# Optimization experiments

Measured on AMD Instinct MI355X. Metric: run time of the kernel, lower is better.

## Reference

```python
import jax, jax.numpy as jnp
import numpy as np

NQ = 8
DIM = 2 ** NQ  # 256 amplitudes
HALF_PI = float(np.pi / 2)

CNOT_M = jnp.array([[1, 0, 0, 0], [0, 1, 0, 0], [0, 0, 0, 1], [0, 0, 1, 0]], dtype=jnp.complex64)
SWAP_M = jnp.array([[1, 0, 0, 0], [0, 0, 1, 0], [0, 1, 0, 0], [0, 0, 0, 1]], dtype=jnp.complex64)

# PauliZ sign vectors per wire; wire 0 is the most-significant bit (PennyLane convention)
_bits = (np.arange(DIM)[None, :] >> (NQ - 1 - np.arange(NQ))[:, None]) & 1
ZSIGNS = jnp.asarray(1.0 - 2.0 * _bits, dtype=jnp.float32)  # [NQ, DIM]


def _rx(t):
    c = jnp.cos(0.5 * t).astype(jnp.complex64)
    s = (-1j * jnp.sin(0.5 * t)).astype(jnp.complex64)
    return jnp.stack([jnp.stack([c, s]), jnp.stack([s, c])])


def _ry(t):
    c = jnp.cos(0.5 * t).astype(jnp.complex64)
    s = jnp.sin(0.5 * t).astype(jnp.complex64)
    return jnp.stack([jnp.stack([c, -s]), jnp.stack([s, c])])


def _rz(t):
    e0 = jnp.exp(-0.5j * t).astype(jnp.complex64)
    e1 = jnp.exp(0.5j * t).astype(jnp.complex64)
    z = jnp.zeros((), jnp.complex64)
    return jnp.stack([jnp.stack([e0, z]), jnp.stack([z, e1])])


def _ixx(t):
    c = jnp.cos(0.5 * t).astype(jnp.complex64)
    s = (-1j * jnp.sin(0.5 * t)).astype(jnp.complex64)
    z = jnp.zeros((), jnp.complex64)
    return jnp.stack([jnp.stack([c, z, z, s]), jnp.stack([z, c, s, z]),
                      jnp.stack([z, s, c, z]), jnp.stack([s, z, z, c])])


def _apply_1q(psi, U, w):
    # psi: [B] + [2]*NQ ; apply 2x2 U on wire w
    psi = jnp.moveaxis(psi, 1 + w, -1)
    psi = psi @ U.T
    return jnp.moveaxis(psi, -1, 1 + w)


def _apply_2q(psi, U, w1, w2):
    # apply 4x4 U on wires (w1, w2); w1 is the more-significant wire of U
    psi = jnp.moveaxis(psi, (1 + w1, 1 + w2), (-2, -1))
    shp = psi.shape
    psi = (psi.reshape(shp[:-2] + (4,)) @ U.T).reshape(shp)
    return jnp.moveaxis(psi, (-2, -1), (1 + w1, 1 + w2))


def _edges_from_coupling(coupling):
    # Mirrors the torch code: threshold min-max normalized coupling at 0.5.
    # This is a non-differentiable, data-dependent circuit-structure decision,
    # so it is resolved on concrete values (as the Python ifs do in torch).
    c = np.asarray(jax.device_get(coupling), dtype=np.float64)
    cn = (c - c.min()) / (c.max() - c.min())
    adj = cn > 0.5
    return [(i, j) for i in range(NQ) for j in range(i + 1, NQ) if adj[i, j]]


def _conv(psi, i, j, p):
    psi = _apply_1q(psi, _rz(jnp.float32(-HALF_PI)), j)
    psi = _apply_2q(psi, CNOT_M, j, i)  # CNOT control=j target=i
    psi = _apply_1q(psi, _rz(p[0]), i)
    psi = _apply_1q(psi, _ry(p[1]), j)
    psi = _apply_2q(psi, CNOT_M, i, j)
    psi = _apply_1q(psi, _ry(p[2]), j)
    psi = _apply_2q(psi, CNOT_M, j, i)
    psi = _apply_1q(psi, _rz(jnp.float32(HALF_PI)), i)
    return psi


def _pool(psi, i, j, p):
    psi = _apply_1q(psi, _rz(jnp.float32(-HALF_PI)), j)
    psi = _apply_2q(psi, CNOT_M, j, i)
    psi = _apply_1q(psi, _rz(p[0]), i)
    psi = _apply_1q(psi, _ry(p[1]), j)
    psi = _apply_2q(psi, CNOT_M, i, j)
    psi = _apply_1q(psi, _ry(p[2]), j)
    return psi


def _circuit(x, weights, coupling, edges):
    B = x.shape[0]
    # AmplitudeEmbedding(normalize=True)
    psi = (x / jnp.linalg.norm(x, axis=1, keepdims=True)).astype(jnp.complex64)
    psi = psi.reshape((B,) + (2,) * NQ)
    for i in range(NQ):
        psi = _apply_1q(psi, _rx(weights[i]), i)
        psi = _apply_1q(psi, _ry(weights[i + NQ]), i)
        psi = _apply_1q(psi, _rz(weights[i + 2 * NQ]), i)
    for i in range(NQ):
        for j in range(i + 1, NQ):
            psi = _apply_2q(psi, _ixx(coupling[i, j]), i, j)
    widx = 3 * NQ
    for (i, j) in edges:
        nonadjacent = abs(i - j) != 1
        if nonadjacent:
            psi = _apply_2q(psi, SWAP_M, i, j)
        psi = _conv(psi, i, j, weights[widx:widx + 3])
        psi = _pool(psi, i, j, weights[widx + 3:widx + 6])
        widx += 6
        if nonadjacent:
            psi = _apply_2q(psi, SWAP_M, i, j)
    psi_f = psi.reshape(B, DIM)
    probs = psi_f.real ** 2 + psi_f.imag ** 2  # [B, DIM]
    return probs @ ZSIGNS.T  # [B, NQ] expval(PauliZ(i))


def setup_inputs() -> dict:
    B = 65536
    key = jax.random.key(0)
    k1, k2, k3 = jax.random.split(key, 3)
    x = jax.random.normal(k1, (B, DIM), dtype=jnp.float32)
    weights = jax.random.normal(k2, (3 * NQ + 6 * 28,), dtype=jnp.float32)  # 192: max edges = C(8,2)=28
    coupling = jax.random.normal(k3, (NQ, NQ), dtype=jnp.float32)
    return {"x": x, "weights": weights, "coupling": coupling}


def reference(x, weights, coupling):
    edges = _edges_from_coupling(coupling)
    return _circuit(x, weights, coupling, edges)
```

## Files before the change

### kernel.cpp

```cpp
#include <hip/hip_runtime.h>

#define HP 1.57079632679489662f

typedef float f32x4 __attribute__((ext_vector_type(4)));
typedef short sh4 __attribute__((ext_vector_type(4)));
typedef __bf16 bf16x8 __attribute__((ext_vector_type(8)));

__device__ __forceinline__ unsigned short f2bf(float f) {
  unsigned int u = __builtin_bit_cast(unsigned int, f);
  u += 0x7fffu + ((u >> 16) & 1u);
  return (unsigned short)(u >> 16);
}

__device__ __forceinline__ void rowswap4(float (&mr)[4][4], float (&mi)[4][4], int a, int b) {
#pragma unroll
  for (int c = 0; c < 4; c++) {
    float tr = mr[a][c]; mr[a][c] = mr[b][c]; mr[b][c] = tr;
    float ti = mi[a][c]; mi[a][c] = mi[b][c]; mi[b][c] = ti;
  }
}

__device__ __forceinline__ void absorb_rz(float (&mr)[4][4], float (&mi)[4][4], float t, int bitpos) {
  float ch = cosf(0.5f * t), sh = sinf(0.5f * t);
#pragma unroll
  for (int r = 0; r < 4; r++) {
    float ph = ((r >> bitpos) & 1) ? sh : -sh;
#pragma unroll
    for (int c = 0; c < 4; c++) {
      float ar = mr[r][c], ai = mi[r][c];
      mr[r][c] = ch * ar - ph * ai;
      mi[r][c] = ch * ai + ph * ar;
    }
  }
}

__device__ __forceinline__ void absorb_ry(float (&mr)[4][4], float (&mi)[4][4], float t, int bitpos) {
  float ch = cosf(0.5f * t), sh = sinf(0.5f * t);
#pragma unroll
  for (int r = 0; r < 4; r++) {
    if ((r >> bitpos) & 1) continue;
    int rb = r | (1 << bitpos);
#pragma unroll
    for (int c = 0; c < 4; c++) {
      float ar = mr[r][c], ai = mi[r][c];
      float br = mr[rb][c], bi = mi[rb][c];
      mr[r][c]  = ch * ar - sh * br;  mi[r][c]  = ch * ai - sh * bi;
      mr[rb][c] = sh * ar + ch * br;  mi[rb][c] = sh * ai + ch * bi;
    }
  }
}


__global__ __launch_bounds__(256) void build_u_kernel(const float* __restrict__ wt,
                                                      const float* __restrict__ coup,
                                                      void* __restrict__ wsv) {
  unsigned char* Ub = (unsigned char*)wsv + 4096;
  const int c = blockIdx.x;
  const int tid = threadIdx.x;

  __shared__ float2 s[256];
  __shared__ float Q1s[64];
  __shared__ float E4s[28 * 32];
  __shared__ int metas[57];

  {
    double mn = 1e300, mx = -1e300;
    for (int k = 0; k < 64; k++) {
      double v = (double)coup[k];
      mn = v < mn ? v : mn;
      mx = v > mx ? v : mx;
    }
    int cnt = 0, myi = -1, myj = -1;
    for (int i = 0; i < 8; i++)
      for (int j = i + 1; j < 8; j++) {
        double cn = ((double)coup[i * 8 + j] - mn) / (mx - mn);
        if (cn > 0.5) {
          if (cnt == tid) { myi = i; myj = j; }
          cnt++;
        }
      }
    if (tid == 0) metas[0] = cnt;

    if (tid < 8) {
      float tx = wt[tid], ty = wt[8 + tid], tz = wt[16 + tid];
      float cx = cosf(0.5f * tx), sx = sinf(0.5f * tx);
      float cy = cosf(0.5f * ty), sy = sinf(0.5f * ty);
      float cz = cosf(0.5f * tz), sz = sinf(0.5f * tz);
      float m00r = cy * cx,  m00i = sy * sx;
      float m01r = -sy * cx, m01i = -cy * sx;
      float m10r = sy * cx,  m10i = -cy * sx;
      float m11r = cy * cx,  m11i = -sy * sx;
      float* q = Q1s + tid * 8;
      q[0] = cz * m00r + sz * m00i; q[1] = cz * m00i - sz * m00r;
      q[2] = cz * m01r + sz * m01i; q[3] = cz * m01i - sz * m01r;
      q[4] = cz * m10r - sz * m10i; q[5] = cz * m10i + sz * m10r;
      q[6] = cz * m11r - sz * m11i; q[7] = cz * m11i + sz * m11r;
    }

    if (tid < cnt && tid < 28) {
      float mr[4][4], mi[4][4];
#pragma unroll
      for (int r = 0; r < 4; r++)
#pragma unroll
        for (int cc = 0; cc < 4; cc++) { mr[r][cc] = (r == cc) ? 1.f : 0.f; mi[r][cc] = 0.f; }

      bool nonadj = (myj - myi) != 1;
      int wb = 24 + 6 * tid;

      if (nonadj) rowswap4(mr, mi, 1, 2);
      absorb_rz(mr, mi, -HP, 0);
      rowswap4(mr, mi, 1, 3);
      absorb_rz(mr, mi, wt[wb + 0], 1);
      absorb_ry(mr, mi, wt[wb + 1], 0);
      rowswap4(mr, mi, 2, 3);
      absorb_ry(mr, mi, wt[wb + 2], 0);
      rowswap4(mr, mi, 1, 3);
      absorb_rz(mr, mi, HP, 1);
      absorb_rz(mr, mi, -HP, 0);
      rowswap4(mr, mi, 1, 3);
      absorb_rz(mr, mi, wt[wb + 3], 1);
      absorb_ry(mr, mi, wt[wb + 4], 0);
      rowswap4(mr, mi, 2, 3);
      absorb_ry(mr, mi, wt[wb + 5], 0);
      if (nonadj) rowswap4(mr, mi, 1, 2);

      float* e = E4s + tid * 32;
#pragma unroll
      for (int r = 0; r < 4; r++)
#pragma unroll
        for (int cc = 0; cc < 4; cc++) {
          e[(r * 4 + cc) * 2]     = mr[r][cc];
          e[(r * 4 + cc) * 2 + 1] = mi[r][cc];
        }
      metas[1 + 2 * tid] = myi;
      metas[2 + 2 * tid] = myj;
    }
  }

  s[tid] = make_float2(tid == c ? 1.f : 0.f, 0.f);
  __syncthreads();

  for (int wi = 0; wi < 8; wi++) {
    const float* M = Q1s + wi * 8;
    int p = 7 - wi;
    float2 a0 = s[tid & ~(1 << p)];
    float2 a1 = s[tid | (1 << p)];
    int b = (tid >> p) & 1;
    float m0r = M[(b * 2 + 0) * 2], m0i = M[(b * 2 + 0) * 2 + 1];
    float m1r = M[(b * 2 + 1) * 2], m1i = M[(b * 2 + 1) * 2 + 1];
    float nr = m0r * a0.x - m0i * a0.y + m1r * a1.x - m1i * a1.y;
    float ni = m0r * a0.y + m0i * a0.x + m1r * a1.y + m1i * a1.x;
    __syncthreads();
    s[tid] = make_float2(nr, ni);
    __syncthreads();
  }

  for (int i = 0; i < 8; i++)
    for (int j = i + 1; j < 8; j++) {
      float t = coup[i * 8 + j];
      float ch = cosf(0.5f * t), sn = sinf(0.5f * t);
      int mask = (1 << (7 - i)) | (1 << (7 - j));
      float2 a = s[tid];
      float2 b = s[tid ^ mask];
      __syncthreads();
      s[tid] = make_float2(ch * a.x + sn * b.y, ch * a.y - sn * b.x);
      __syncthreads();
    }

  int ne = metas[0];
  for (int e = 0; e < ne; e++) {
    int i = metas[1 + 2 * e], j = metas[2 + 2 * e];
    int p1 = 7 - i, p2 = 7 - j;
    int m1 = 1 << p1, m2 = 1 << p2;
    int b = ((tid >> p1) & 1) * 2 + ((tid >> p2) & 1);
    int base = tid & ~(m1 | m2);
    float2 a0 = s[base];
    float2 a1 = s[base | m2];
    float2 a2 = s[base | m1];
    float2 a3 = s[base | m1 | m2];
    const float* M = E4s + e * 32 + b * 8;
    float nr = M[0] * a0.x - M[1] * a0.y + M[2] * a1.x - M[3] * a1.y
             + M[4] * a2.x - M[5] * a2.y + M[6] * a3.x - M[7] * a3.y;
    float ni = M[0] * a0.y + M[1] * a0.x + M[2] * a1.y + M[3] * a1.x
             + M[4] * a2.y + M[5] * a2.x + M[6] * a3.y + M[7] * a3.x;
    __syncthreads();
    s[tid] = make_float2(nr, ni);
    __syncthreads();
  }

  {
    int ks = c >> 5, kc = c & 31;
    int sb = (kc >> 4) & 1, lg2 = (kc >> 2) & 3, ii = kc & 3;
    int p = (lg2 + tid) & 3;
    unsigned char* base = Ub + (size_t)ks * 32768 + (size_t)(2 * tid) * 64 + p * 16 + sb * 8 + ii * 2;
    *(unsigned short*)(base)      = f2bf(s[tid].x);
    *(unsigned short*)(base + 64) = f2bf(s[tid].y);
  }
}

#define MFMA_STEP(KS, AREG)                                                              \
  {                                                                                      \
    uint4 bq[4];                                                                         \
    _Pragma("unroll")                                                                    \
    for (int nf = 0; nf < 4; nf++) {                                                     \
      const int n = nf * 16 + lm;                                                        \
      int byte = (n * 512 + (KS) * 64 + lg * 16) ^ ((n & 7) << 4);                       \
      bq[nf] = *reinterpret_cast<const uint4*>(&smem[byte]);                             \
    }                                                                                    \
    __builtin_amdgcn_s_setprio(1);                                                       \
    _Pragma("unroll")                                                                    \
    for (int mf = 0; mf < 4; mf++) {                                                     \
      const sh4 alo = __builtin_bit_cast(sh4, make_uint2(AREG[mf].x, AREG[mf].y));       \
      const sh4 ahi = __builtin_bit_cast(sh4, make_uint2(AREG[mf].z, AREG[mf].w));       \
      _Pragma("unroll")                                                                  \
      for (int nf = 0; nf < 4; nf++) {                                                   \
        const sh4 blo = __builtin_bit_cast(sh4, make_uint2(bq[nf].x, bq[nf].y));         \
        const sh4 bhi = __builtin_bit_cast(sh4, make_uint2(bq[nf].z, bq[nf].w));         \
        acc[mf][nf] = __builtin_amdgcn_mfma_f32_16x16x16bf16_1k(alo, blo, acc[mf][nf], 0, 0, 0); \
        acc[mf][nf] = __builtin_amdgcn_mfma_f32_16x16x16bf16_1k(ahi, bhi, acc[mf][nf], 0, 0, 0); \
      }                                                                                  \
    }                                                                                    \
    __builtin_amdgcn_s_setprio(0);                                                       \
  }

__global__ __launch_bounds__(512, 4) void gemm_l2(const float* __restrict__ x,
                                                  const void* __restrict__ wsv,
                                                  float* __restrict__ out) {
  const unsigned char* Ub = (const unsigned char*)wsv + 4096;
  __shared__ __align__(16) unsigned char smem[32768];

  const int tid = threadIdx.x;
  const int tile = blockIdx.x;
  const int wv = tid >> 6;
  const int lane = tid & 63;
  const int lm = lane & 15;
  const int lg = lane >> 4;

  const unsigned char* abase[4];
#pragma unroll
  for (int mf = 0; mf < 4; mf++) {
    const int m = wv * 64 + mf * 16 + lm;
    const int p = (lg + (m >> 1)) & 3;
    abase[mf] = Ub + (size_t)m * 64 + p * 16;
  }
  uint4 aP[4], aQ[4];
#pragma unroll
  for (int mf = 0; mf < 4; mf++) aP[mf] = *reinterpret_cast<const uint4*>(abase[mf]);

  {
    const int rl = tid >> 3;
    const int seg = tid & 7;
    const float4* xs = (const float4*)(x + (size_t)(tile * 64 + rl) * 256 + seg * 32);
    float4 v[8];
    float ss = 0.f;
#pragma unroll
    for (int i = 0; i < 8; i++) {
      v[i] = xs[i];
      ss += v[i].x * v[i].x + v[i].y * v[i].y + v[i].z * v[i].z + v[i].w * v[i].w;
    }
    ss += __shfl_xor(ss, 1);
    ss += __shfl_xor(ss, 2);
    ss += __shfl_xor(ss, 4);
    float inv = 1.0f / sqrtf(ss);
    const float* vf = (const float*)v;
#pragma unroll
    for (int u = 0; u < 4; u++) {
      bf16x8 w;
#pragma unroll
      for (int j = 0; j < 8; j++)
        w[j] = (__bf16)(vf[16 * (j >> 2) + 4 * u + (j & 3)] * inv);
      uint4 pack = __builtin_bit_cast(uint4, w);
      int byte = (rl * 512 + seg * 64 + u * 16) ^ ((rl & 7) << 4);
      *reinterpret_cast<uint4*>(&smem[byte]) = pack;
    }
  }

  f32x4 acc[4][4] = {};
  __syncthreads();

#pragma unroll
  for (int kk = 0; kk < 4; kk++) {
#pragma unroll
    for (int mf = 0; mf < 4; mf++)
      aQ[mf] = *reinterpret_cast<const uint4*>(abase[mf] + (size_t)(2 * kk + 1) * 32768);
    MFMA_STEP(2 * kk, aP);
    if (kk < 3) {
#pragma unroll
      for (int mf = 0; mf < 4; mf++)
        aP[mf] = *reinterpret_cast<const uint4*>(abase[mf] + (size_t)(2 * kk + 2) * 32768);
    }
    MFMA_STEP(2 * kk + 1, aQ);
  }
  __syncthreads();

  float pq[4][8];
#pragma unroll
  for (int nf = 0; nf < 4; nf++) {
    float T = 0.f, S7 = 0.f, S4 = 0.f, S3 = 0.f;
#pragma unroll
    for (int mf = 0; mf < 4; mf++) {
      f32x4 a = acc[mf][nf];
      float p0 = a[0] * a[0] + a[1] * a[1];
      float p1 = a[2] * a[2] + a[3] * a[3];
      float sp = p0 + p1, d = p0 - p1;
      T += sp;
      S7 += d;
      S4 += (mf & 1) ? -sp : sp;
      S3 += (mf & 2) ? -sp : sp;
    }
    pq[nf][7] = S7;
    pq[nf][6] = (lg & 1) ? -T : T;
    pq[nf][5] = (lg & 2) ? -T : T;
    pq[nf][4] = S4;
    pq[nf][3] = S3;
    pq[nf][2] = (wv & 1) ? -T : T;
    pq[nf][1] = (wv & 2) ? -T : T;
    pq[nf][0] = (wv & 4) ? -T : T;
  }
#pragma unroll
  for (int nf = 0; nf < 4; nf++)
#pragma unroll
    for (int k = 0; k < 8; k++) {
      pq[nf][k] += __shfl_xor(pq[nf][k], 16);
      pq[nf][k] += __shfl_xor(pq[nf][k], 32);
    }

  float* part = (float*)smem;
  if (lg == 0) {
#pragma unroll
    for (int nf = 0; nf < 4; nf++) {
      float* dst = part + (wv * 64 + nf * 16 + lm) * 8;
#pragma unroll
      for (int k = 0; k < 8; k++) dst[k] = pq[nf][k];
    }
  }
  __syncthreads();
  {
    int b = tid >> 3, q = tid & 7;
    float v2 = 0.f;
#pragma unroll
    for (int w2 = 0; w2 < 8; w2++) v2 += part[(w2 * 64 + b) * 8 + q];
    out[(size_t)(tile * 64 + b) * 8 + q] = v2;
  }
}

extern "C" void kernel_launch(void* const* d_in, const int* in_sizes, int n_in,
                              void* d_out, int out_size, void* d_ws, size_t ws_size,
                              hipStream_t stream) {
  const float* x    = (const float*)d_in[0];
  const float* wt   = (const float*)d_in[1];
  const float* coup = (const float*)d_in[2];
  float* out = (float*)d_out;

  build_u_kernel<<<256, 256, 0, stream>>>(wt, coup, d_ws);
  gemm_l2<<<1024, 512, 0, stream>>>(x, d_ws, out);
}
```

Baseline: 58.57 us.

## Run unitary build in one wave with shuffles; rotate K-chunk order in GEMM

New measurement: 70.69 us. +20.7%, slower.

```diff
diff --git a/kernel.cpp b/kernel.cpp
--- a/kernel.cpp
+++ b/kernel.cpp
@@ -51,14 +51,13 @@
 }
 
 
-__global__ __launch_bounds__(256) void build_u_kernel(const float* __restrict__ wt,
-                                                      const float* __restrict__ coup,
-                                                      void* __restrict__ wsv) {
+__global__ __launch_bounds__(64) void build_u_wave(const float* __restrict__ wt,
+                                                   const float* __restrict__ coup,
+                                                   void* __restrict__ wsv) {
   unsigned char* Ub = (unsigned char*)wsv + 4096;
   const int c = blockIdx.x;
-  const int tid = threadIdx.x;
-
-  __shared__ float2 s[256];
+  const int lane = threadIdx.x;
+
   __shared__ float Q1s[64];
   __shared__ float E4s[28 * 32];
   __shared__ int metas[57];
@@ -75,14 +74,14 @@
       for (int j = i + 1; j < 8; j++) {
         double cn = ((double)coup[i * 8 + j] - mn) / (mx - mn);
         if (cn > 0.5) {
-          if (cnt == tid) { myi = i; myj = j; }
+          if (cnt == lane) { myi = i; myj = j; }
           cnt++;
         }
       }
-    if (tid == 0) metas[0] = cnt;
-
-    if (tid < 8) {
-      float tx = wt[tid], ty = wt[8 + tid], tz = wt[16 + tid];
+    if (lane == 0) metas[0] = cnt;
+
+    if (lane < 8) {
+      float tx = wt[lane], ty = wt[8 + lane], tz = wt[16 + lane];
       float cx = cosf(0.5f * tx), sx = sinf(0.5f * tx);
       float cy = cosf(0.5f * ty), sy = sinf(0.5f * ty);
       float cz = cosf(0.5f * tz), sz = sinf(0.5f * tz);
@@ -90,14 +89,14 @@
       float m01r = -sy * cx, m01i = -cy * sx;
       float m10r = sy * cx,  m10i = -cy * sx;
       float m11r = cy * cx,  m11i = -sy * sx;
-      float* q = Q1s + tid * 8;
+      float* q = Q1s + lane * 8;
       q[0] = cz * m00r + sz * m00i; q[1] = cz * m00i - sz * m00r;
       q[2] = cz * m01r + sz * m01i; q[3] = cz * m01i - sz * m01r;
       q[4] = cz * m10r - sz * m10i; q[5] = cz * m10i + sz * m10r;
       q[6] = cz * m11r - sz * m11i; q[7] = cz * m11i + sz * m11r;
     }
 
-    if (tid < cnt && tid < 28) {
+    if (lane < cnt && lane < 28) {
       float mr[4][4], mi[4][4];
 #pragma unroll
       for (int r = 0; r < 4; r++)
@@ -105,7 +104,7 @@
         for (int cc = 0; cc < 4; cc++) { mr[r][cc] = (r == cc) ? 1.f : 0.f; mi[r][cc] = 0.f; }
 
       bool nonadj = (myj - myi) != 1;
-      int wb = 24 + 6 * tid;
+      int wb = 24 + 6 * lane;
 
       if (nonadj) rowswap4(mr, mi, 1, 2);
       absorb_rz(mr, mi, -HP, 0);
@@ -124,7 +123,7 @@
       absorb_ry(mr, mi, wt[wb + 5], 0);
       if (nonadj) rowswap4(mr, mi, 1, 2);
 
-      float* e = E4s + tid * 32;
+      float* e = E4s + lane * 32;
 #pragma unroll
       for (int r = 0; r < 4; r++)
 #pragma unroll
@@ -132,27 +131,51 @@
           e[(r * 4 + cc) * 2]     = mr[r][cc];
           e[(r * 4 + cc) * 2 + 1] = mi[r][cc];
         }
-      metas[1 + 2 * tid] = myi;
-      metas[2 + 2 * tid] = myj;
-    }
-  }
-
-  s[tid] = make_float2(tid == c ? 1.f : 0.f, 0.f);
+      metas[1 + 2 * lane] = myi;
+      metas[2 + 2 * lane] = myj;
+    }
+  }
   __syncthreads();
+
+  float2 st[4];
+#pragma unroll
+  for (int q = 0; q < 4; q++)
+    st[q] = make_float2((q * 64 + lane) == c ? 1.f : 0.f, 0.f);
+
+  auto partner = [&](int M, float2 (&par)[4]) {
+    const int qm = M >> 6, lm = M & 63;
+    float2 t0, t1, t2, t3;
+    if (qm == 0)      { t0 = st[0]; t1 = st[1]; t2 = st[2]; t3 = st[3]; }
+    else if (qm == 1) { t0 = st[1]; t1 = st[0]; t2 = st[3]; t3 = st[2]; }
+    else if (qm == 2) { t0 = st[2]; t1 = st[3]; t2 = st[0]; t3 = st[1]; }
+    else              { t0 = st[3]; t1 = st[2]; t2 = st[1]; t3 = st[0]; }
+    if (lm) {
+      t0.x = __shfl_xor(t0.x, lm); t0.y = __shfl_xor(t0.y, lm);
+      t1.x = __shfl_xor(t1.x, lm); t1.y = __shfl_xor(t1.y, lm);
+      t2.x = __shfl_xor(t2.x, lm); t2.y = __shfl_xor(t2.y, lm);
+      t3.x = __shfl_xor(t3.x, lm); t3.y = __shfl_xor(t3.y, lm);
+    }
+    par[0] = t0; par[1] = t1; par[2] = t2; par[3] = t3;
+  };
 
   for (int wi = 0; wi < 8; wi++) {
     const float* M = Q1s + wi * 8;
-    int p = 7 - wi;
-    float2 a0 = s[tid & ~(1 << p)];
-    float2 a1 = s[tid | (1 << p)];
-    int b = (tid >> p) & 1;
-    float m0r = M[(b * 2 + 0) * 2], m0i = M[(b * 2 + 0) * 2 + 1];
-    float m1r = M[(b * 2 + 1) * 2], m1i = M[(b * 2 + 1) * 2 + 1];
-    float nr = m0r * a0.x - m0i * a0.y + m1r * a1.x - m1i * a1.y;
-    float ni = m0r * a0.y + m0i * a0.x + m1r * a1.y + m1i * a1.x;
-    __syncthreads();
-    s[tid] = make_float2(nr, ni);
-    __syncthreads();
+    const int p = 7 - wi;
+    float2 par[4];
+    partner(1 << p, par);
+    float m00r = M[0], m00i = M[1], m01r = M[2], m01i = M[3];
+    float m10r = M[4], m10i = M[5], m11r = M[6], m11i = M[7];
+#pragma unroll
+    for (int q = 0; q < 4; q++) {
+      int b = ((q * 64 + lane) >> p) & 1;
+      float2 own = st[q], pr = par[q];
+      float2 x0 = b ? pr : own;
+      float2 x1 = b ? own : pr;
+      float c0r = b ? m10r : m00r, c0i = b ? m10i : m00i;
+      float c1r = b ? m11r : m01r, c1i = b ? m11i : m01i;
+      st[q].x = c0r * x0.x - c0i * x0.y + c1r * x1.x - c1i * x1.y;
+      st[q].y = c0r * x0.y + c0i * x0.x + c1r * x1.y + c1i * x1.x;
+    }
   }
 
   for (int i = 0; i < 8; i++)
@@ -160,11 +183,13 @@
       float t = coup[i * 8 + j];
       float ch = cosf(0.5f * t), sn = sinf(0.5f * t);
       int mask = (1 << (7 - i)) | (1 << (7 - j));
-      float2 a = s[tid];
-      float2 b = s[tid ^ mask];
-      __syncthreads();
-      s[tid] = make_float2(ch * a.x + sn * b.y, ch * a.y - sn * b.x);
-      __syncthreads();
+      float2 par[4];
+      partner(mask, par);
+#pragma unroll
+      for (int q = 0; q < 4; q++) {
+        float2 own = st[q], pr = par[q];
+        st[q] = make_float2(ch * own.x + sn * pr.y, ch * own.y - sn * pr.x);
+      }
     }
 
   int ne = metas[0];
@@ -172,29 +197,39 @@
     int i = metas[1 + 2 * e], j = metas[2 + 2 * e];
     int p1 = 7 - i, p2 = 7 - j;
     int m1 = 1 << p1, m2 = 1 << p2;
-    int b = ((tid >> p1) & 1) * 2 + ((tid >> p2) & 1);
-    int base = tid & ~(m1 | m2);
-    float2 a0 = s[base];
-    float2 a1 = s[base | m2];
-    float2 a2 = s[base | m1];
-    float2 a3 = s[base | m1 | m2];
-    const float* M = E4s + e * 32 + b * 8;
-    float nr = M[0] * a0.x - M[1] * a0.y + M[2] * a1.x - M[3] * a1.y
-             + M[4] * a2.x - M[5] * a2.y + M[6] * a3.x - M[7] * a3.y;
-    float ni = M[0] * a0.y + M[1] * a0.x + M[2] * a1.y + M[3] * a1.x
-             + M[4] * a2.y + M[5] * a2.x + M[6] * a3.y + M[7] * a3.x;
-    __syncthreads();
-    s[tid] = make_float2(nr, ni);
-    __syncthreads();
+    float2 pa2[4], pa1[4], pa12[4];
+    partner(m2, pa2);
+    partner(m1, pa1);
+    partner(m1 | m2, pa12);
+    const float* E = E4s + e * 32;
+#pragma unroll
+    for (int q = 0; q < 4; q++) {
+      int r = q * 64 + lane;
+      int b = ((r >> p1) & 1) * 2 + ((r >> p2) & 1);
+      float nr = 0.f, ni = 0.f;
+      { float Mr = E[(b * 4 + b) * 2], Mi = E[(b * 4 + b) * 2 + 1];
+        nr += Mr * st[q].x - Mi * st[q].y; ni += Mr * st[q].y + Mi * st[q].x; }
+      { int t2 = b ^ 1; float Mr = E[(b * 4 + t2) * 2], Mi = E[(b * 4 + t2) * 2 + 1];
+        nr += Mr * pa2[q].x - Mi * pa2[q].y; ni += Mr * pa2[q].y + Mi * pa2[q].x; }
+      { int t2 = b ^ 2; float Mr = E[(b * 4 + t2) * 2], Mi = E[(b * 4 + t2) * 2 + 1];
+        nr += Mr * pa1[q].x - Mi * pa1[q].y; ni += Mr * pa1[q].y + Mi * pa1[q].x; }
+      { int t2 = b ^ 3; float Mr = E[(b * 4 + t2) * 2], Mi = E[(b * 4 + t2) * 2 + 1];
+        nr += Mr * pa12[q].x - Mi * pa12[q].y; ni += Mr * pa12[q].y + Mi * pa12[q].x; }
+      st[q] = make_float2(nr, ni);
+    }
   }
 
   {
     int ks = c >> 5, kc = c & 31;
     int sb = (kc >> 4) & 1, lg2 = (kc >> 2) & 3, ii = kc & 3;
-    int p = (lg2 + tid) & 3;
-    unsigned char* base = Ub + (size_t)ks * 32768 + (size_t)(2 * tid) * 64 + p * 16 + sb * 8 + ii * 2;
-    *(unsigned short*)(base)      = f2bf(s[tid].x);
-    *(unsigned short*)(base + 64) = f2bf(s[tid].y);
+#pragma unroll
+    for (int q = 0; q < 4; q++) {
+      int r = q * 64 + lane;
+      int p = (lg2 + r) & 3;
+      unsigned char* base = Ub + (size_t)ks * 32768 + (size_t)(2 * r) * 64 + p * 16 + sb * 8 + ii * 2;
+      *(unsigned short*)(base)      = f2bf(st[q].x);
+      *(unsigned short*)(base + 64) = f2bf(st[q].y);
+    }
   }
 }
 
@@ -235,6 +270,7 @@
   const int lane = tid & 63;
   const int lm = lane & 15;
   const int lg = lane >> 4;
+  const int rot = (blockIdx.x >> 3) & 7;
 
   const unsigned char* abase[4];
 #pragma unroll
@@ -245,7 +281,8 @@
   }
   uint4 aP[4], aQ[4];
 #pragma unroll
-  for (int mf = 0; mf < 4; mf++) aP[mf] = *reinterpret_cast<const uint4*>(abase[mf]);
+  for (int mf = 0; mf < 4; mf++)
+    aP[mf] = *reinterpret_cast<const uint4*>(abase[mf] + (size_t)rot * 32768);
 
   {
     const int rl = tid >> 3;
@@ -280,16 +317,19 @@
 
 #pragma unroll
   for (int kk = 0; kk < 4; kk++) {
+    const int c0 = (2 * kk + rot) & 7;
+    const int c1 = (2 * kk + 1 + rot) & 7;
 #pragma unroll
     for (int mf = 0; mf < 4; mf++)
-      aQ[mf] = *reinterpret_cast<const uint4*>(abase[mf] + (size_t)(2 * kk + 1) * 32768);
-    MFMA_STEP(2 * kk, aP);
+      aQ[mf] = *reinterpret_cast<const uint4*>(abase[mf] + (size_t)c1 * 32768);
+    MFMA_STEP(c0, aP);
     if (kk < 3) {
+      const int c2 = (2 * kk + 2 + rot) & 7;
 #pragma unroll
       for (int mf = 0; mf < 4; mf++)
-        aP[mf] = *reinterpret_cast<const uint4*>(abase[mf] + (size_t)(2 * kk + 2) * 32768);
-    }
-    MFMA_STEP(2 * kk + 1, aQ);
+        aP[mf] = *reinterpret_cast<const uint4*>(abase[mf] + (size_t)c2 * 32768);
+    }
+    MFMA_STEP(c1, aQ);
   }
   __syncthreads();
 
@@ -352,6 +392,6 @@
   const float* coup = (const float*)d_in[2];
   float* out = (float*)d_out;
 
-  build_u_kernel<<<256, 256, 0, stream>>>(wt, coup, d_ws);
+  build_u_wave<<<256, 64, 0, stream>>>(wt, coup, d_ws);
   gemm_l2<<<1024, 512, 0, stream>>>(x, d_ws, out);
 }
```

## Process two batch tiles per GEMM block and build unitary with single-wave blocks

Applied to the files above, without the earlier changes.

Result: slower. 74.33 us (+26.9%).

```diff
diff --git a/kernel.cpp b/kernel.cpp
--- a/kernel.cpp
+++ b/kernel.cpp
@@ -51,12 +51,12 @@
 }
 
 
-__global__ __launch_bounds__(256) void build_u_kernel(const float* __restrict__ wt,
-                                                      const float* __restrict__ coup,
-                                                      void* __restrict__ wsv) {
+__global__ __launch_bounds__(64) void build_u_wave(const float* __restrict__ wt,
+                                                   const float* __restrict__ coup,
+                                                   void* __restrict__ wsv) {
   unsigned char* Ub = (unsigned char*)wsv + 4096;
   const int c = blockIdx.x;
-  const int tid = threadIdx.x;
+  const int lane = threadIdx.x;
 
   __shared__ float2 s[256];
   __shared__ float Q1s[64];
@@ -75,14 +75,14 @@
       for (int j = i + 1; j < 8; j++) {
         double cn = ((double)coup[i * 8 + j] - mn) / (mx - mn);
         if (cn > 0.5) {
-          if (cnt == tid) { myi = i; myj = j; }
+          if (cnt == lane) { myi = i; myj = j; }
           cnt++;
         }
       }
-    if (tid == 0) metas[0] = cnt;
-
-    if (tid < 8) {
-      float tx = wt[tid], ty = wt[8 + tid], tz = wt[16 + tid];
+    if (lane == 0) metas[0] = cnt;
+
+    if (lane < 8) {
+      float tx = wt[lane], ty = wt[8 + lane], tz = wt[16 + lane];
       float cx = cosf(0.5f * tx), sx = sinf(0.5f * tx);
       float cy = cosf(0.5f * ty), sy = sinf(0.5f * ty);
       float cz = cosf(0.5f * tz), sz = sinf(0.5f * tz);
@@ -90,14 +90,14 @@
       float m01r = -sy * cx, m01i = -cy * sx;
       float m10r = sy * cx,  m10i = -cy * sx;
       float m11r = cy * cx,  m11i = -sy * sx;
-      float* q = Q1s + tid * 8;
+      float* q = Q1s + lane * 8;
       q[0] = cz * m00r + sz * m00i; q[1] = cz * m00i - sz * m00r;
       q[2] = cz * m01r + sz * m01i; q[3] = cz * m01i - sz * m01r;
       q[4] = cz * m10r - sz * m10i; q[5] = cz * m10i + sz * m10r;
       q[6] = cz * m11r - sz * m11i; q[7] = cz * m11i + sz * m11r;
     }
 
-    if (tid < cnt && tid < 28) {
+    if (lane < cnt && lane < 28) {
       float mr[4][4], mi[4][4];
 #pragma unroll
       for (int r = 0; r < 4; r++)
@@ -105,7 +105,7 @@
         for (int cc = 0; cc < 4; cc++) { mr[r][cc] = (r == cc) ? 1.f : 0.f; mi[r][cc] = 0.f; }
 
       bool nonadj = (myj - myi) != 1;
-      int wb = 24 + 6 * tid;
+      int wb = 24 + 6 * lane;
 
       if (nonadj) rowswap4(mr, mi, 1, 2);
       absorb_rz(mr, mi, -HP, 0);
@@ -124,7 +124,7 @@
       absorb_ry(mr, mi, wt[wb + 5], 0);
       if (nonadj) rowswap4(mr, mi, 1, 2);
 
-      float* e = E4s + tid * 32;
+      float* e = E4s + lane * 32;
 #pragma unroll
       for (int r = 0; r < 4; r++)
 #pragma unroll
@@ -132,27 +132,31 @@
           e[(r * 4 + cc) * 2]     = mr[r][cc];
           e[(r * 4 + cc) * 2 + 1] = mi[r][cc];
         }
-      metas[1 + 2 * tid] = myi;
-      metas[2 + 2 * tid] = myj;
-    }
-  }
-
-  s[tid] = make_float2(tid == c ? 1.f : 0.f, 0.f);
-  __syncthreads();
+      metas[1 + 2 * lane] = myi;
+      metas[2 + 2 * lane] = myj;
+    }
+  }
+
+#pragma unroll
+  for (int q = 0; q < 4; q++)
+    s[q * 64 + lane] = make_float2((q * 64 + lane) == c ? 1.f : 0.f, 0.f);
 
   for (int wi = 0; wi < 8; wi++) {
-    const float* M = Q1s + wi * 8;
-    int p = 7 - wi;
-    float2 a0 = s[tid & ~(1 << p)];
-    float2 a1 = s[tid | (1 << p)];
-    int b = (tid >> p) & 1;
-    float m0r = M[(b * 2 + 0) * 2], m0i = M[(b * 2 + 0) * 2 + 1];
-    float m1r = M[(b * 2 + 1) * 2], m1i = M[(b * 2 + 1) * 2 + 1];
-    float nr = m0r * a0.x - m0i * a0.y + m1r * a1.x - m1i * a1.y;
-    float ni = m0r * a0.y + m0i * a0.x + m1r * a1.y + m1i * a1.x;
-    __syncthreads();
-    s[tid] = make_float2(nr, ni);
-    __syncthreads();
+    const int p = 7 - wi;
+    const int m = 1 << p;
+    float2 nw[4];
+#pragma unroll
+    for (int q = 0; q < 4; q++) {
+      int r = q * 64 + lane;
+      int b = (r >> p) & 1;
+      float2 a0 = s[r & ~m];
+      float2 a1 = s[r | m];
+      float4 Mv = *reinterpret_cast<const float4*>(&Q1s[wi * 8 + b * 4]);
+      nw[q].x = Mv.x * a0.x - Mv.y * a0.y + Mv.z * a1.x - Mv.w * a1.y;
+      nw[q].y = Mv.x * a0.y + Mv.y * a0.x + Mv.z * a1.y + Mv.w * a1.x;
+    }
+#pragma unroll
+    for (int q = 0; q < 4; q++) s[q * 64 + lane] = nw[q];
   }
 
   for (int i = 0; i < 8; i++)
@@ -160,11 +164,16 @@
       float t = coup[i * 8 + j];
       float ch = cosf(0.5f * t), sn = sinf(0.5f * t);
       int mask = (1 << (7 - i)) | (1 << (7 - j));
-      float2 a = s[tid];
-      float2 b = s[tid ^ mask];
-      __syncthreads();
-      s[tid] = make_float2(ch * a.x + sn * b.y, ch * a.y - sn * b.x);
-      __syncthreads();
+      float2 nw[4];
+#pragma unroll
+      for (int q = 0; q < 4; q++) {
+        int r = q * 64 + lane;
+        float2 own = s[r];
+        float2 pr = s[r ^ mask];
+        nw[q] = make_float2(ch * own.x + sn * pr.y, ch * own.y - sn * pr.x);
+      }
+#pragma unroll
+      for (int q = 0; q < 4; q++) s[q * 64 + lane] = nw[q];
     }
 
   int ne = metas[0];
@@ -172,39 +181,49 @@
     int i = metas[1 + 2 * e], j = metas[2 + 2 * e];
     int p1 = 7 - i, p2 = 7 - j;
     int m1 = 1 << p1, m2 = 1 << p2;
-    int b = ((tid >> p1) & 1) * 2 + ((tid >> p2) & 1);
-    int base = tid & ~(m1 | m2);
-    float2 a0 = s[base];
-    float2 a1 = s[base | m2];
-    float2 a2 = s[base | m1];
-    float2 a3 = s[base | m1 | m2];
-    const float* M = E4s + e * 32 + b * 8;
-    float nr = M[0] * a0.x - M[1] * a0.y + M[2] * a1.x - M[3] * a1.y
-             + M[4] * a2.x - M[5] * a2.y + M[6] * a3.x - M[7] * a3.y;
-    float ni = M[0] * a0.y + M[1] * a0.x + M[2] * a1.y + M[3] * a1.x
-             + M[4] * a2.y + M[5] * a2.x + M[6] * a3.y + M[7] * a3.x;
-    __syncthreads();
-    s[tid] = make_float2(nr, ni);
-    __syncthreads();
+    float2 nw[4];
+#pragma unroll
+    for (int q = 0; q < 4; q++) {
+      int r = q * 64 + lane;
+      int b = ((r >> p1) & 1) * 2 + ((r >> p2) & 1);
+      int base = r & ~(m1 | m2);
+      float2 a0 = s[base];
+      float2 a1 = s[base | m2];
+      float2 a2 = s[base | m1];
+      float2 a3 = s[base | m1 | m2];
+      float4 M01 = *reinterpret_cast<const float4*>(&E4s[e * 32 + b * 8]);
+      float4 M23 = *reinterpret_cast<const float4*>(&E4s[e * 32 + b * 8 + 4]);
+      nw[q].x = M01.x * a0.x - M01.y * a0.y + M01.z * a1.x - M01.w * a1.y
+              + M23.x * a2.x - M23.y * a2.y + M23.z * a3.x - M23.w * a3.y;
+      nw[q].y = M01.x * a0.y + M01.y * a0.x + M01.z * a1.y + M01.w * a1.x
+              + M23.x * a2.y + M23.y * a2.x + M23.z * a3.y + M23.w * a3.x;
+    }
+#pragma unroll
+    for (int q = 0; q < 4; q++) s[q * 64 + lane] = nw[q];
   }
 
   {
     int ks = c >> 5, kc = c & 31;
     int sb = (kc >> 4) & 1, lg2 = (kc >> 2) & 3, ii = kc & 3;
-    int p = (lg2 + tid) & 3;
-    unsigned char* base = Ub + (size_t)ks * 32768 + (size_t)(2 * tid) * 64 + p * 16 + sb * 8 + ii * 2;
-    *(unsigned short*)(base)      = f2bf(s[tid].x);
-    *(unsigned short*)(base + 64) = f2bf(s[tid].y);
-  }
-}
-
-#define MFMA_STEP(KS, AREG)                                                              \
+#pragma unroll
+    for (int q = 0; q < 4; q++) {
+      int r = q * 64 + lane;
+      int p = (lg2 + r) & 3;
+      unsigned char* base = Ub + (size_t)ks * 32768 + (size_t)(2 * r) * 64 + p * 16 + sb * 8 + ii * 2;
+      float2 a = s[r];
+      *(unsigned short*)(base)      = f2bf(a.x);
+      *(unsigned short*)(base + 64) = f2bf(a.y);
+    }
+  }
+}
+
+#define MFMA_STEP(PSIOFF, KS, AREG)                                                      \
   {                                                                                      \
     uint4 bq[4];                                                                         \
     _Pragma("unroll")                                                                    \
     for (int nf = 0; nf < 4; nf++) {                                                     \
       const int n = nf * 16 + lm;                                                        \
-      int byte = (n * 512 + (KS) * 64 + lg * 16) ^ ((n & 7) << 4);                       \
+      int byte = (PSIOFF) + ((n * 512 + (KS) * 64 + lg * 16) ^ ((n & 7) << 4));          \
       bq[nf] = *reinterpret_cast<const uint4*>(&smem[byte]);                             \
     }                                                                                    \
     __builtin_amdgcn_s_setprio(1);                                                       \
@@ -223,18 +242,123 @@
     __builtin_amdgcn_s_setprio(0);                                                       \
   }
 
-__global__ __launch_bounds__(512, 4) void gemm_l2(const float* __restrict__ x,
-                                                  const void* __restrict__ wsv,
-                                                  float* __restrict__ out) {
+#define KLOOP(PSIOFF)                                                                    \
+  _Pragma("unroll")                                                                      \
+  for (int kk = 0; kk < 4; kk++) {                                                       \
+    _Pragma("unroll")                                                                    \
+    for (int mf = 0; mf < 4; mf++)                                                       \
+      aQ[mf] = *reinterpret_cast<const uint4*>(abase[mf] + (size_t)(2 * kk + 1) * 32768);\
+    MFMA_STEP(PSIOFF, 2 * kk, aP);                                                       \
+    if (kk < 3) {                                                                        \
+      _Pragma("unroll")                                                                  \
+      for (int mf = 0; mf < 4; mf++)                                                     \
+        aP[mf] = *reinterpret_cast<const uint4*>(abase[mf] + (size_t)(2 * kk + 2) * 32768);\
+    }                                                                                    \
+    MFMA_STEP(PSIOFF, 2 * kk + 1, aQ);                                                   \
+  }
+
+#define PACK_PSI(V, PSIOFF)                                                              \
+  {                                                                                      \
+    float ss = 0.f;                                                                      \
+    _Pragma("unroll")                                                                    \
+    for (int i = 0; i < 8; i++)                                                          \
+      ss += V[i].x * V[i].x + V[i].y * V[i].y + V[i].z * V[i].z + V[i].w * V[i].w;       \
+    ss += __shfl_xor(ss, 1);                                                             \
+    ss += __shfl_xor(ss, 2);                                                             \
+    ss += __shfl_xor(ss, 4);                                                             \
+    float inv = 1.0f / sqrtf(ss);                                                        \
+    const float* vf = (const float*)V;                                                   \
+    _Pragma("unroll")                                                                    \
+    for (int u = 0; u < 4; u++) {                                                        \
+      bf16x8 w;                                                                          \
+      _Pragma("unroll")                                                                  \
+      for (int j = 0; j < 8; j++)                                                        \
+        w[j] = (__bf16)(vf[16 * (j >> 2) + 4 * u + (j & 3)] * inv);                      \
+      uint4 pack = __builtin_bit_cast(uint4, w);                                         \
+      int byte = (PSIOFF) + ((rl * 512 + seg * 64 + u * 16) ^ ((rl & 7) << 4));          \
+      *reinterpret_cast<uint4*>(&smem[byte]) = pack;                                     \
+    }                                                                                    \
+  }
+
+#define EPILOGUE(TILE)                                                                   \
+  {                                                                                      \
+    float pq[4][8];                                                                      \
+    _Pragma("unroll")                                                                    \
+    for (int nf = 0; nf < 4; nf++) {                                                     \
+      float T = 0.f, S7 = 0.f, S4 = 0.f, S3 = 0.f;                                       \
+      _Pragma("unroll")                                                                  \
+      for (int mf = 0; mf < 4; mf++) {                                                   \
+        f32x4 a = acc[mf][nf];                                                           \
+        float p0 = a[0] * a[0] + a[1] * a[1];                                            \
+        float p1 = a[2] * a[2] + a[3] * a[3];                                            \
+        float sp = p0 + p1, d = p0 - p1;                                                 \
+        T += sp;                                                                         \
+        S7 += d;                                                                         \
+        S4 += (mf & 1) ? -sp : sp;                                                       \
+        S3 += (mf & 2) ? -sp : sp;                                                       \
+      }                                                                                  \
+      pq[nf][7] = S7;                                                                    \
+      pq[nf][6] = (lg & 1) ? -T : T;                                                     \
+      pq[nf][5] = (lg & 2) ? -T : T;                                                     \
+      pq[nf][4] = S4;                                                                    \
+      pq[nf][3] = S3;                                                                    \
+      pq[nf][2] = (wv & 1) ? -T : T;                                                     \
+      pq[nf][1] = (wv & 2) ? -T : T;                                                     \
+      pq[nf][0] = (wv & 4) ? -T : T;                                                     \
+    }                                                                                    \
+    _Pragma("unroll")                                                                    \
+    for (int nf = 0; nf < 4; nf++)                                                       \
+      _Pragma("unroll")                                                                  \
+      for (int k = 0; k < 8; k++) {                                                      \
+        pq[nf][k] += __shfl_xor(pq[nf][k], 16);                                          \
+        pq[nf][k] += __shfl_xor(pq[nf][k], 32);                                          \
+      }                                                                                  \
+    float* part = (float*)smem;                                                          \
+    if (lg == 0) {                                                                       \
+      _Pragma("unroll")                                                                  \
+      for (int nf = 0; nf < 4; nf++) {                                                   \
+        float* dst = part + (wv * 64 + nf * 16 + lm) * 8;                                \
+        _Pragma("unroll")                                                                \
+        for (int k = 0; k < 8; k++) dst[k] = pq[nf][k];                                  \
+      }                                                                                  \
+    }                                                                                    \
+    __syncthreads();                                                                     \
+    {                                                                                    \
+      int b = tid >> 3, q = tid & 7;                                                     \
+      float v2 = 0.f;                                                                    \
+      _Pragma("unroll")                                                                  \
+      for (int w2 = 0; w2 < 8; w2++) v2 += part[(w2 * 64 + b) * 8 + q];                  \
+      out[(size_t)((TILE) * 64 + b) * 8 + q] = v2;                                       \
+    }                                                                                    \
+    __syncthreads();                                                                     \
+  }
+
+__global__ __launch_bounds__(512, 2) void gemm2(const float* __restrict__ x,
+                                                const void* __restrict__ wsv,
+                                                float* __restrict__ out) {
   const unsigned char* Ub = (const unsigned char*)wsv + 4096;
-  __shared__ __align__(16) unsigned char smem[32768];
+  __shared__ __align__(16) unsigned char smem[65536];
+  const int PSI1 = 32768;
 
   const int tid = threadIdx.x;
-  const int tile = blockIdx.x;
+  const int bid = blockIdx.x;
   const int wv = tid >> 6;
   const int lane = tid & 63;
   const int lm = lane & 15;
   const int lg = lane >> 4;
+  const int rl = tid >> 3;
+  const int seg = tid & 7;
+
+  const int tile0 = bid * 2;
+  const int tile1 = bid * 2 + 1;
+
+  const float4* xs0 = (const float4*)(x + (size_t)(tile0 * 64 + rl) * 256 + seg * 32);
+  const float4* xs1 = (const float4*)(x + (size_t)(tile1 * 64 + rl) * 256 + seg * 32);
+  float4 v0[8], v1[8];
+#pragma unroll
+  for (int i = 0; i < 8; i++) v0[i] = xs0[i];
+#pragma unroll
+  for (int i = 0; i < 8; i++) v1[i] = xs1[i];
 
   const unsigned char* abase[4];
 #pragma unroll
@@ -247,101 +371,29 @@
 #pragma unroll
   for (int mf = 0; mf < 4; mf++) aP[mf] = *reinterpret_cast<const uint4*>(abase[mf]);
 
-  {
-    const int rl = tid >> 3;
-    const int seg = tid & 7;
-    const float4* xs = (const float4*)(x + (size_t)(tile * 64 + rl) * 256 + seg * 32);
-    float4 v[8];
-    float ss = 0.f;
-#pragma unroll
-    for (int i = 0; i < 8; i++) {
-      v[i] = xs[i];
-      ss += v[i].x * v[i].x + v[i].y * v[i].y + v[i].z * v[i].z + v[i].w * v[i].w;
-    }
-    ss += __shfl_xor(ss, 1);
-    ss += __shfl_xor(ss, 2);
-    ss += __shfl_xor(ss, 4);
-    float inv = 1.0f / sqrtf(ss);
-    const float* vf = (const float*)v;
-#pragma unroll
-    for (int u = 0; u < 4; u++) {
-      bf16x8 w;
-#pragma unroll
-      for (int j = 0; j < 8; j++)
-        w[j] = (__bf16)(vf[16 * (j >> 2) + 4 * u + (j & 3)] * inv);
-      uint4 pack = __builtin_bit_cast(uint4, w);
-      int byte = (rl * 512 + seg * 64 + u * 16) ^ ((rl & 7) << 4);
-      *reinterpret_cast<uint4*>(&smem[byte]) = pack;
-    }
-  }
+  PACK_PSI(v0, 0);
 
   f32x4 acc[4][4] = {};
   __syncthreads();
 
-#pragma unroll
-  for (int kk = 0; kk < 4; kk++) {
-#pragma unroll
-    for (int mf = 0; mf < 4; mf++)
-      aQ[mf] = *reinterpret_cast<const uint4*>(abase[mf] + (size_t)(2 * kk + 1) * 32768);
-    MFMA_STEP(2 * kk, aP);
-    if (kk < 3) {
-#pragma unroll
-      for (int mf = 0; mf < 4; mf++)
-        aP[mf] = *reinterpret_cast<const uint4*>(abase[mf] + (size_t)(2 * kk + 2) * 32768);
-    }
-    MFMA_STEP(2 * kk + 1, aQ);
-  }
+  KLOOP(0);
+
+  PACK_PSI(v1, PSI1);
+#pragma unroll
+  for (int mf = 0; mf < 4; mf++) aP[mf] = *reinterpret_cast<const uint4*>(abase[mf]);
+
   __syncthreads();
 
-  float pq[4][8];
-#pragma unroll
-  for (int nf = 0; nf < 4; nf++) {
-    float T = 0.f, S7 = 0.f, S4 = 0.f, S3 = 0.f;
-#pragma unroll
-    for (int mf = 0; mf < 4; mf++) {
-      f32x4 a = acc[mf][nf];
-      float p0 = a[0] * a[0] + a[1] * a[1];
-      float p1 = a[2] * a[2] + a[3] * a[3];
-      float sp = p0 + p1, d = p0 - p1;
-      T += sp;
-      S7 += d;
-      S4 += (mf & 1) ? -sp : sp;
-      S3 += (mf & 2) ? -sp : sp;
-    }
-    pq[nf][7] = S7;
-    pq[nf][6] = (lg & 1) ? -T : T;
-    pq[nf][5] = (lg & 2) ? -T : T;
-    pq[nf][4] = S4;
-    pq[nf][3] = S3;
-    pq[nf][2] = (wv & 1) ? -T : T;
-    pq[nf][1] = (wv & 2) ? -T : T;
-    pq[nf][0] = (wv & 4) ? -T : T;
-  }
-#pragma unroll
-  for (int nf = 0; nf < 4; nf++)
-#pragma unroll
-    for (int k = 0; k < 8; k++) {
-      pq[nf][k] += __shfl_xor(pq[nf][k], 16);
-      pq[nf][k] += __shfl_xor(pq[nf][k], 32);
-    }
-
-  float* part = (float*)smem;
-  if (lg == 0) {
-#pragma unroll
-    for (int nf = 0; nf < 4; nf++) {
-      float* dst = part + (wv * 64 + nf * 16 + lm) * 8;
-#pragma unroll
-      for (int k = 0; k < 8; k++) dst[k] = pq[nf][k];
-    }
-  }
+  EPILOGUE(tile0);
+
+#pragma unroll
+  for (int mf = 0; mf < 4; mf++)
+#pragma unroll
+    for (int nf = 0; nf < 4; nf++) acc[mf][nf] = (f32x4){0.f, 0.f, 0.f, 0.f};
+
+  KLOOP(PSI1);
   __syncthreads();
-  {
-    int b = tid >> 3, q = tid & 7;
-    float v2 = 0.f;
-#pragma unroll
-    for (int w2 = 0; w2 < 8; w2++) v2 += part[(w2 * 64 + b) * 8 + q];
-    out[(size_t)(tile * 64 + b) * 8 + q] = v2;
-  }
+  EPILOGUE(tile1);
 }
 
 extern "C" void kernel_launch(void* const* d_in, const int* in_sizes, int n_in,
@@ -352,6 +404,6 @@
   const float* coup = (const float*)d_in[2];
   float* out = (float*)d_out;
 
-  build_u_kernel<<<256, 256, 0, stream>>>(wt, coup, d_ws);
-  gemm_l2<<<1024, 512, 0, stream>>>(x, d_ws, out);
-}
+  build_u_wave<<<256, 64, 0, stream>>>(wt, coup, d_ws);
+  gemm2<<<512, 512, 0, stream>>>(x, d_ws, out);
+}
```
